# Performance work log

Measured on AMD Instinct MI355X. Metric: run time of the kernel, lower is better.

The kernel has to match this reference:

```python
import jax, jax.numpy as jnp
import numpy as np
import math

B, L, H, NH, DH = 2, 2048, 1024, 16, 64  # batch, seq, hidden, heads, head dim


def setup_inputs() -> dict:
    key = jax.random.key(0)
    ks = jax.random.split(key, 12)
    s = 0.02
    return {
        "v": jax.random.normal(ks[0], (B, L, H), jnp.float32),
        "k": jax.random.normal(ks[1], (B, L, H), jnp.float32),
        "q": jax.random.normal(ks[2], (B, L, H), jnp.float32),
        "mask": jnp.zeros((B, 1, 1, L), jnp.bool_),
        "Wv": jax.random.normal(ks[3], (H, H), jnp.float32) * s,
        "bv": jnp.zeros((H,), jnp.float32),
        "Wk": jax.random.normal(ks[4], (H, H), jnp.float32) * s,
        "bk": jnp.zeros((H,), jnp.float32),
        "Wq": jax.random.normal(ks[5], (H, H), jnp.float32) * s,
        "bq": jnp.zeros((H,), jnp.float32),
        "Wt": jax.random.normal(ks[6], (H, 1), jnp.float32) * s,
        "bt": jnp.zeros((1,), jnp.float32),
        "Wm": jax.random.normal(ks[7], (H, H), jnp.float32) * s,
        "bm": jnp.zeros((H,), jnp.float32),
    }


def reference(v, k, q, mask, Wv, bv, Wk, bk, Wq, bq, Wt, bt, Wm, bm):
    vp = (v @ Wv + bv).reshape(B, L, NH, DH).transpose(0, 2, 1, 3)  # [B,NH,L,DH]
    kp = k @ Wk + bk  # [B,L,H]
    qp = q @ Wq + bq  # [B,L,H]
    threshold = (qp * kp) @ Wt + bt  # [B,L,1] learned per-position gate threshold
    kh = kp.reshape(B, L, NH, DH).transpose(0, 2, 1, 3)  # [B,NH,L,DH]
    qh = qp.reshape(B, L, NH, DH).transpose(0, 2, 1, 3)
    scores = jnp.einsum("bhqd,bhkd->bhqk", qh, kh) / math.sqrt(DH)
    scores = jnp.where(mask, -1e9, scores)
    att_map = jax.nn.softmax(scores, axis=-1)  # [B,NH,Lq,Lk]
    # column sums: over queries (axis -2) then over heads -> [B,Lk,1]
    colsum = att_map.sum(axis=2).sum(axis=1)[..., None]
    a = (colsum - threshold) > 0  # [B,L,1] boolean gate
    atted = jnp.einsum("bhqk,bhkd->bhqd", att_map, vp)  # [B,NH,L,DH]
    atted = atted.transpose(0, 2, 1, 3).reshape(B, L, H)
    atted = atted * a.astype(atted.dtype)
    return atted @ Wm + bm
```

## Files before the change

### kernel.cpp

```cpp
#include <hip/hip_runtime.h>
#include <math.h>

#define BATCH 2
#define SEQ   2048
#define HID   1024
#define NHEAD 16
#define DHEAD 64
#define MROWS (BATCH*SEQ)
#define QK_SCALE 0.125f

typedef __attribute__((ext_vector_type(8))) short short8;
typedef __attribute__((ext_vector_type(4))) short short4v;
typedef __attribute__((ext_vector_type(4))) float floatx4;
#define MFMA16(a,b,c) __builtin_amdgcn_mfma_f32_16x16x32_bf16(a,b,c,0,0,0)

__device__ __forceinline__ unsigned short f2bf(float x) {
    union { float f; unsigned u; } v; v.f = x;
    return (unsigned short)((v.u + 0x8000u) >> 16);
}
__device__ __forceinline__ float bf2f(unsigned short s) {
    union { unsigned u; float f; } v; v.u = ((unsigned)s) << 16;
    return v.f;
}
__device__ __forceinline__ unsigned pack_bf16(float lo, float hi) {
    union { float f; unsigned u; } a, b; a.f = lo; b.f = hi;
    return __builtin_amdgcn_perm(b.u + 0x8000u, a.u + 0x8000u, 0x07060302u);
}

__global__ __launch_bounds__(256) void cvt_bf16_kernel(
    const float* __restrict__ i0, const float* __restrict__ i1,
    const float* __restrict__ i2,
    unsigned short* __restrict__ o0, unsigned short* __restrict__ o1,
    unsigned short* __restrict__ o2)
{
    const float* in; unsigned short* out;
    switch (blockIdx.y) {
        case 0:  in = i0; out = o0; break;
        case 1:  in = i1; out = o1; break;
        default: in = i2; out = o2; break;
    }
    const size_t i = ((size_t)blockIdx.x * 256 + threadIdx.x) * 8;
    const float4 a = *(const float4*)&in[i];
    const float4 b = *(const float4*)&in[i + 4];
    uint4 u;
    u.x = pack_bf16(a.x, a.y); u.y = pack_bf16(a.z, a.w);
    u.z = pack_bf16(b.x, b.y); u.w = pack_bf16(b.z, b.w);
    *(uint4*)&out[i] = u;
}

__global__ __launch_bounds__(256) void wtrans_kernel(
    const float* __restrict__ W0, const float* __restrict__ W1,
    const float* __restrict__ W2, const float* __restrict__ W3,
    unsigned short* __restrict__ T0, unsigned short* __restrict__ T1,
    unsigned short* __restrict__ T2, unsigned short* __restrict__ T3)
{
    const float* W; unsigned short* Wt;
    switch (blockIdx.z) {
        case 0: W = W0; Wt = T0; break;
        case 1: W = W1; Wt = T1; break;
        case 2: W = W2; Wt = T2; break;
        default: W = W3; Wt = T3; break;
    }
    __shared__ float T[64][68];
    const int tid = threadIdx.x;
    const int k0 = blockIdx.x * 64, n0 = blockIdx.y * 64;
#pragma unroll
    for (int it = 0; it < 4; it++) {
        const int id = it * 256 + tid;
        const int r = id >> 4, c4 = (id & 15) << 2;
        *(float4*)&T[r][c4] = *(const float4*)&W[(size_t)(k0 + r) * HID + n0 + c4];
    }
    __syncthreads();
#pragma unroll
    for (int it = 0; it < 2; it++) {
        const int id = it * 256 + tid;
        const int n = id >> 3, k8 = (id & 7) << 3;
        uint4 u;
        u.x = pack_bf16(T[k8 + 0][n], T[k8 + 1][n]);
        u.y = pack_bf16(T[k8 + 2][n], T[k8 + 3][n]);
        u.z = pack_bf16(T[k8 + 4][n], T[k8 + 5][n]);
        u.w = pack_bf16(T[k8 + 6][n], T[k8 + 7][n]);
        *(uint4*)&Wt[(size_t)(n0 + n) * HID + k0 + k8] = u;
    }
}

__global__ __launch_bounds__(256) void vtrans_kernel(
    const unsigned short* __restrict__ vb, unsigned short* __restrict__ vt)
{
    __shared__ unsigned short T[64][72];
    const int b = blockIdx.z, h = blockIdx.y, l0 = blockIdx.x * 64;
    const int tid = threadIdx.x;
#pragma unroll
    for (int it = 0; it < 2; it++) {
        const int id = it * 256 + tid;
        const int l = id >> 3, c8 = (id & 7) << 3;
        *(uint4*)&T[l][c8] =
            *(const uint4*)&vb[(size_t)(b * SEQ + l0 + l) * HID + h * DHEAD + c8];
    }
    __syncthreads();
#pragma unroll
    for (int it = 0; it < 2; it++) {
        const int id = it * 256 + tid;
        const int d = id >> 3, l8 = (id & 7) << 3;
        ushort4 u0, u1;
        u0.x = T[l8 + 0][d]; u0.y = T[l8 + 1][d];
        u0.z = T[l8 + 2][d]; u0.w = T[l8 + 3][d];
        u1.x = T[l8 + 4][d]; u1.y = T[l8 + 5][d];
        u1.z = T[l8 + 6][d]; u1.w = T[l8 + 7][d];
        const size_t o = ((size_t)(b * NHEAD + h) * DHEAD + d) * SEQ + l0 + l8;
        *(ushort4*)&vt[o] = u0;
        *(ushort4*)&vt[o + 4] = u1;
    }
}

__global__ __launch_bounds__(256) void gemm_mfma_kernel(
    const unsigned short* __restrict__ Ab, const unsigned short* __restrict__ Bt,
    const float* __restrict__ bias,
    const float* __restrict__ gate_cs, const float* __restrict__ gate_th,
    float* __restrict__ Cf, unsigned short* __restrict__ Cb,
    int M, int N, int K)
{
    __shared__ unsigned short As[128][72];
    __shared__ unsigned short Bs[128][72];
    const int tid = threadIdx.x;
    const int w = tid >> 6, lane = tid & 63;
    const int c = lane & 15, quad = lane >> 4;
    const int m0 = blockIdx.x * 128, n0 = blockIdx.y * 128;
    const int wm = (w >> 1) * 64, wn = (w & 1) * 64;

    bool grow[4] = {true, true, true, true};
    if (gate_cs) {
#pragma unroll
        for (int it = 0; it < 4; it++) {
            const int r = (it * 256 + tid) >> 3;
            grow[it] = (gate_cs[m0 + r] - gate_th[m0 + r]) > 0.f;
        }
    }

    floatx4 acc[4][4];
#pragma unroll
    for (int i = 0; i < 4; i++)
#pragma unroll
        for (int j = 0; j < 4; j++) acc[i][j] = (floatx4){0.f, 0.f, 0.f, 0.f};

    for (int kc = 0; kc < K; kc += 64) {
        __syncthreads();
#pragma unroll
        for (int it = 0; it < 4; it++) {
            const int id = it * 256 + tid;
            const int r = id >> 3, c8 = (id & 7) << 3;
            uint4 u = *(const uint4*)&Ab[(size_t)(m0 + r) * K + kc + c8];
            if (!grow[it]) { u.x = 0; u.y = 0; u.z = 0; u.w = 0; }
            *(uint4*)&As[r][c8] = u;
            *(uint4*)&Bs[r][c8] = *(const uint4*)&Bt[(size_t)(n0 + r) * K + kc + c8];
        }
        __syncthreads();
#pragma unroll
        for (int kk = 0; kk < 2; kk++) {
            short8 af[4], bf[4];
#pragma unroll
            for (int mt = 0; mt < 4; mt++)
                af[mt] = *(const short8*)&As[wm + mt * 16 + c][kk * 32 + quad * 8];
#pragma unroll
            for (int nt = 0; nt < 4; nt++)
                bf[nt] = *(const short8*)&Bs[wn + nt * 16 + c][kk * 32 + quad * 8];
#pragma unroll
            for (int mt = 0; mt < 4; mt++)
#pragma unroll
                for (int nt = 0; nt < 4; nt++)
                    acc[mt][nt] = MFMA16(af[mt], bf[nt], acc[mt][nt]);
        }
    }

#pragma unroll
    for (int nt = 0; nt < 4; nt++) {
        const int n = n0 + wn + nt * 16 + c;
        const float bb = bias[n];
#pragma unroll
        for (int mt = 0; mt < 4; mt++) {
            const int m = m0 + wm + mt * 16 + quad * 4;
#pragma unroll
            for (int r = 0; r < 4; r++) {
                const float val = acc[mt][nt][r] + bb;
                const size_t off = (size_t)(m + r) * N + n;
                if (Cf) Cf[off] = val;
                if (Cb) Cb[off] = f2bf(val);
            }
        }
    }
}

__global__ __launch_bounds__(256) void threshold_kernel(
    const unsigned short* __restrict__ qb, const unsigned short* __restrict__ kb,
    const float* __restrict__ Wt, const float* __restrict__ bt,
    float* __restrict__ thr)
{
    const int w = threadIdx.x >> 6, lane = threadIdx.x & 63;
    const int row = blockIdx.x * 4 + w;
    const unsigned short* qr = qb + (size_t)row * HID;
    const unsigned short* kr = kb + (size_t)row * HID;
    float s = 0.f;
#pragma unroll
    for (int ii = 0; ii < 2; ii++) {
        const int base = ii * 512 + lane * 8;
        const ushort4 q0 = *(const ushort4*)&qr[base];
        const ushort4 q1 = *(const ushort4*)&qr[base + 4];
        const ushort4 k0 = *(const ushort4*)&kr[base];
        const ushort4 k1 = *(const ushort4*)&kr[base + 4];
        const float4 w0 = *(const float4*)&Wt[base];
        const float4 w1 = *(const float4*)&Wt[base + 4];
        s += bf2f(q0.x) * bf2f(k0.x) * w0.x + bf2f(q0.y) * bf2f(k0.y) * w0.y +
             bf2f(q0.z) * bf2f(k0.z) * w0.z + bf2f(q0.w) * bf2f(k0.w) * w0.w +
             bf2f(q1.x) * bf2f(k1.x) * w1.x + bf2f(q1.y) * bf2f(k1.y) * w1.y +
             bf2f(q1.z) * bf2f(k1.z) * w1.z + bf2f(q1.w) * bf2f(k1.w) * w1.w;
    }
#pragma unroll
    for (int off = 32; off > 0; off >>= 1) s += __shfl_xor(s, off, 64);
    if (lane == 0) thr[row] = s + bt[0];
}

__global__ __launch_bounds__(512) void flash_mfma_kernel(
    const unsigned short* __restrict__ qb, const unsigned short* __restrict__ kb,
    const unsigned short* __restrict__ vt, const unsigned char* __restrict__ mask,
    unsigned short* __restrict__ att, float* __restrict__ zinv_out)
{
    const int b = blockIdx.z, h = blockIdx.y;
    const int q0 = blockIdx.x * 128;
    const int tid = threadIdx.x;
    const int w = tid >> 6, lane = tid & 63;
    const int c = lane & 15, quad = lane >> 4;

    __shared__ unsigned short Qs[128][72];
    __shared__ unsigned short Ks[64][72];
    __shared__ unsigned short Vs[64][72];
    __shared__ unsigned short Ps[8][16][68];
    __shared__ float mbf[64];

    const size_t hoff = (size_t)h * DHEAD;
#pragma unroll
    for (int it = 0; it < 2; it++) {
        const int g = it * 512 + tid;
        const int r = g >> 3, c8 = (g & 7) << 3;
        *(uint4*)&Qs[r][c8] =
            *(const uint4*)&qb[(size_t)(b * SEQ + q0 + r) * HID + hoff + c8];
    }
    __syncthreads();
    const short8 aq0 = *(const short8*)&Qs[w * 16 + c][quad * 8];
    const short8 aq1 = *(const short8*)&Qs[w * 16 + c][32 + quad * 8];

    floatx4 acc_o[4];
#pragma unroll
    for (int dt = 0; dt < 4; dt++) acc_o[dt] = (floatx4){0.f, 0.f, 0.f, 0.f};
    float zp[4] = {0.f, 0.f, 0.f, 0.f};
    const size_t vtbase = (size_t)(b * NHEAD + h) * DHEAD * SEQ;

    for (int kc = 0; kc < SEQ; kc += 64) {
        __syncthreads();
        {
            const int r = tid >> 3, c8 = (tid & 7) << 3;
            *(uint4*)&Ks[r][c8] =
                *(const uint4*)&kb[(size_t)(b * SEQ + kc + r) * HID + hoff + c8];
            *(uint4*)&Vs[r][c8] =
                *(const uint4*)&vt[vtbase + (size_t)r * SEQ + kc + c8];
        }
        if (tid < 64) mbf[tid] = mask[(size_t)b * SEQ + kc + tid] ? -1e9f : 0.f;
        __syncthreads();

#pragma unroll
        for (int nt = 0; nt < 4; nt++) {
            const short8 bk0 = *(const short8*)&Ks[nt * 16 + c][quad * 8];
            const short8 bk1 = *(const short8*)&Ks[nt * 16 + c][32 + quad * 8];
            floatx4 s = (floatx4){0.f, 0.f, 0.f, 0.f};
            s = MFMA16(aq0, bk0, s);
            s = MFMA16(aq1, bk1, s);
            const float mb = mbf[nt * 16 + c];
#pragma unroll
            for (int r = 0; r < 4; r++) {
                const float p = __expf(fmaf(s[r], QK_SCALE, mb));
                zp[r] += p;
                Ps[w][quad * 4 + r][nt * 16 + c] = f2bf(p);
            }
        }

        short4v p00 = *(const short4v*)&Ps[w][c][quad * 8];
        short4v p01 = *(const short4v*)&Ps[w][c][quad * 8 + 4];
        short4v p10 = *(const short4v*)&Ps[w][c][32 + quad * 8];
        short4v p11 = *(const short4v*)&Ps[w][c][32 + quad * 8 + 4];
        const short8 ap0 = __builtin_shufflevector(p00, p01, 0, 1, 2, 3, 4, 5, 6, 7);
        const short8 ap1 = __builtin_shufflevector(p10, p11, 0, 1, 2, 3, 4, 5, 6, 7);
#pragma unroll
        for (int dt = 0; dt < 4; dt++) {
            const short8 bv0 = *(const short8*)&Vs[dt * 16 + c][quad * 8];
            const short8 bv1 = *(const short8*)&Vs[dt * 16 + c][32 + quad * 8];
            acc_o[dt] = MFMA16(ap0, bv0, acc_o[dt]);
            acc_o[dt] = MFMA16(ap1, bv1, acc_o[dt]);
        }
    }

#pragma unroll
    for (int r = 0; r < 4; r++) {
        float z = zp[r];
        z += __shfl_xor(z, 1, 64); z += __shfl_xor(z, 2, 64);
        z += __shfl_xor(z, 4, 64); z += __shfl_xor(z, 8, 64);
        zp[r] = 1.0f / (z + 1e-30f);
    }

#pragma unroll
    for (int dt = 0; dt < 4; dt++)
#pragma unroll
        for (int r = 0; r < 4; r++)
            att[(size_t)(b * SEQ + q0 + w * 16 + quad * 4 + r) * HID + hoff +
                dt * 16 + c] = f2bf(acc_o[dt][r] * zp[r]);

    if (c == 0) {
        const size_t zb = (size_t)(b * NHEAD + h) * SEQ + q0 + w * 16 + quad * 4;
#pragma unroll
        for (int r = 0; r < 4; r++) zinv_out[zb + r] = zp[r];
    }
}

__global__ __launch_bounds__(512) void colsum_mfma_kernel(
    const unsigned short* __restrict__ qb, const unsigned short* __restrict__ kb,
    const unsigned char* __restrict__ mask, const float* __restrict__ zinv,
    float* __restrict__ colsum)
{
    const int b = blockIdx.z, h = blockIdx.y, k0 = blockIdx.x * 128;
    const int tid = threadIdx.x;
    const int w = tid >> 6, lane = tid & 63;
    const int c = lane & 15, quad = lane >> 4;

    __shared__ unsigned short Ks[128][72];
    __shared__ unsigned short Qs[64][72];
    __shared__ float zs[64];

    const size_t hoff = (size_t)h * DHEAD;
#pragma unroll
    for (int it = 0; it < 2; it++) {
        const int g = it * 512 + tid;
        const int r = g >> 3, c8 = (g & 7) << 3;
        *(uint4*)&Ks[r][c8] =
            *(const uint4*)&kb[(size_t)(b * SEQ + k0 + r) * HID + hoff + c8];
    }
    float mb[4];
#pragma unroll
    for (int r = 0; r < 4; r++)
        mb[r] = mask[(size_t)b * SEQ + k0 + w * 16 + quad * 4 + r] ? -1e9f : 0.f;
    __syncthreads();
    const short8 ak0 = *(const short8*)&Ks[w * 16 + c][quad * 8];
    const short8 ak1 = *(const short8*)&Ks[w * 16 + c][32 + quad * 8];

    float cs[4] = {0.f, 0.f, 0.f, 0.f};
    const size_t zbase = (size_t)(b * NHEAD + h) * SEQ;

    for (int qc = 0; qc < SEQ; qc += 64) {
        __syncthreads();
        {
            const int r = tid >> 3, c8 = (tid & 7) << 3;
            *(uint4*)&Qs[r][c8] =
                *(const uint4*)&qb[(size_t)(b * SEQ + qc + r) * HID + hoff + c8];
        }
        if (tid < 64) zs[tid] = zinv[zbase + qc + tid];
        __syncthreads();

#pragma unroll
        for (int qt = 0; qt < 4; qt++) {
            const short8 bq0 = *(const short8*)&Qs[qt * 16 + c][quad * 8];
            const short8 bq1 = *(const short8*)&Qs[qt * 16 + c][32 + quad * 8];
            floatx4 s = (floatx4){0.f, 0.f, 0.f, 0.f};
            s = MFMA16(ak0, bq0, s);
            s = MFMA16(ak1, bq1, s);
            const float zi = zs[qt * 16 + c];
#pragma unroll
            for (int r = 0; r < 4; r++)
                cs[r] += __expf(fmaf(s[r], QK_SCALE, mb[r])) * zi;
        }
    }

#pragma unroll
    for (int r = 0; r < 4; r++) {
        float v = cs[r];
        v += __shfl_xor(v, 1, 64); v += __shfl_xor(v, 2, 64);
        v += __shfl_xor(v, 4, 64); v += __shfl_xor(v, 8, 64);
        if (c == 0)
            atomicAdd(&colsum[(size_t)b * SEQ + k0 + w * 16 + quad * 4 + r], v);
    }
}

extern "C" void kernel_launch(void* const* d_in, const int* in_sizes, int n_in,
                              void* d_out, int out_size, void* d_ws, size_t ws_size,
                              hipStream_t stream)
{
    const float* v  = (const float*)d_in[0];
    const float* k  = (const float*)d_in[1];
    const float* q  = (const float*)d_in[2];
    const unsigned char* mask = (const unsigned char*)d_in[3];
    const float* Wv = (const float*)d_in[4];
    const float* bv = (const float*)d_in[5];
    const float* Wk = (const float*)d_in[6];
    const float* bk = (const float*)d_in[7];
    const float* Wq = (const float*)d_in[8];
    const float* bq = (const float*)d_in[9];
    const float* Wt = (const float*)d_in[10];
    const float* bt = (const float*)d_in[11];
    const float* Wm = (const float*)d_in[12];
    const float* bm = (const float*)d_in[13];
    float* out = (float*)d_out;

    const size_t NE = (size_t)MROWS * HID;
    const size_t WE = (size_t)HID * HID;
    unsigned short* qa   = (unsigned short*)d_ws;
    unsigned short* ka   = qa  + NE;
    unsigned short* va   = ka  + NE;
    unsigned short* qp   = va  + NE;
    unsigned short* kp   = qp  + NE;
    unsigned short* vp   = kp  + NE;
    unsigned short* WqT  = vp  + NE;
    unsigned short* WkT  = WqT + WE;
    unsigned short* WvT  = WkT + WE;
    unsigned short* WmT  = WvT + WE;
    float* thr    = (float*)(WmT + WE);
    float* zinv   = thr  + MROWS;
    float* colsum = zinv + (size_t)BATCH * NHEAD * SEQ;
    unsigned short* attb = qa;
    unsigned short* vtb  = ka;

    wtrans_kernel<<<dim3(HID / 64, HID / 64, 4), 256, 0, stream>>>(
        Wq, Wk, Wv, Wm, WqT, WkT, WvT, WmT);

    cvt_bf16_kernel<<<dim3((unsigned)(NE / (256 * 8)), 3), 256, 0, stream>>>(
        q, k, v, qa, ka, va);

    const dim3 gg(MROWS / 128, HID / 128);
    gemm_mfma_kernel<<<gg, 256, 0, stream>>>(qa, WqT, bq, nullptr, nullptr,
                                             nullptr, qp, MROWS, HID, HID);
    gemm_mfma_kernel<<<gg, 256, 0, stream>>>(ka, WkT, bk, nullptr, nullptr,
                                             nullptr, kp, MROWS, HID, HID);
    gemm_mfma_kernel<<<gg, 256, 0, stream>>>(va, WvT, bv, nullptr, nullptr,
                                             nullptr, vp, MROWS, HID, HID);

    vtrans_kernel<<<dim3(SEQ / 64, NHEAD, BATCH), 256, 0, stream>>>(vp, vtb);

    threshold_kernel<<<MROWS / 4, 256, 0, stream>>>(qp, kp, Wt, bt, thr);

    flash_mfma_kernel<<<dim3(SEQ / 128, NHEAD, BATCH), 512, 0, stream>>>(
        qp, kp, vtb, mask, attb, zinv);

    hipMemsetAsync(colsum, 0, MROWS * sizeof(float), stream);
    colsum_mfma_kernel<<<dim3(SEQ / 128, NHEAD, BATCH), 512, 0, stream>>>(
        qp, kp, mask, zinv, colsum);

    gemm_mfma_kernel<<<gg, 256, 0, stream>>>(attb, WmT, bm, colsum, thr,
                                             out, nullptr, MROWS, HID, HID);
}
```

Baseline: 340.9 us.

## Prefetch next tiles into registers, remap blocks per XCD, use native exp2

The GEMM, flash-attention and colsum kernels now load the next K/V/Q (and A/B) tile into registers while the current tile is being computed, so global-load latency overlaps the MFMA work. The flash and colsum kernels use a 1D grid with an XCD-aware remap, so blocks for the same (batch, head) land on the same XCD and can share L2 for K/V. The exponentials switch to native exp2 with the log2e factor folded into the scale. In exchange, register pressure rises, which could lower occupancy, and native exp2 is slightly less accurate.

```diff
diff --git a/kernel.cpp b/kernel.cpp
--- a/kernel.cpp
+++ b/kernel.cpp
@@ -8,11 +8,15 @@
 #define DHEAD 64
 #define MROWS (BATCH*SEQ)
 #define QK_SCALE 0.125f
+#define SCALE_LOG2E 0.1803368801111244f
 
 typedef __attribute__((ext_vector_type(8))) short short8;
 typedef __attribute__((ext_vector_type(4))) short short4v;
 typedef __attribute__((ext_vector_type(4))) float floatx4;
 #define MFMA16(a,b,c) __builtin_amdgcn_mfma_f32_16x16x32_bf16(a,b,c,0,0,0)
+
+extern "C" __device__ float __ocml_native_exp2_f32(float);
+#define EXP2F(x) __ocml_native_exp2_f32(x)
 
 __device__ __forceinline__ unsigned short f2bf(float x) {
     union { float f; unsigned u; } v; v.f = x;
@@ -143,18 +147,36 @@
 #pragma unroll
         for (int j = 0; j < 4; j++) acc[i][j] = (floatx4){0.f, 0.f, 0.f, 0.f};
 
+    uint4 ra[4], rb[4];
+#pragma unroll
+    for (int it = 0; it < 4; it++) {
+        const int id = it * 256 + tid;
+        const int r = id >> 3, c8 = (id & 7) << 3;
+        ra[it] = *(const uint4*)&Ab[(size_t)(m0 + r) * K + c8];
+        rb[it] = *(const uint4*)&Bt[(size_t)(n0 + r) * K + c8];
+    }
+
     for (int kc = 0; kc < K; kc += 64) {
         __syncthreads();
 #pragma unroll
         for (int it = 0; it < 4; it++) {
             const int id = it * 256 + tid;
             const int r = id >> 3, c8 = (id & 7) << 3;
-            uint4 u = *(const uint4*)&Ab[(size_t)(m0 + r) * K + kc + c8];
+            uint4 u = ra[it];
             if (!grow[it]) { u.x = 0; u.y = 0; u.z = 0; u.w = 0; }
             *(uint4*)&As[r][c8] = u;
-            *(uint4*)&Bs[r][c8] = *(const uint4*)&Bt[(size_t)(n0 + r) * K + kc + c8];
-        }
-        __syncthreads();
+            *(uint4*)&Bs[r][c8] = rb[it];
+        }
+        __syncthreads();
+        if (kc + 64 < K) {
+#pragma unroll
+            for (int it = 0; it < 4; it++) {
+                const int id = it * 256 + tid;
+                const int r = id >> 3, c8 = (id & 7) << 3;
+                ra[it] = *(const uint4*)&Ab[(size_t)(m0 + r) * K + kc + 64 + c8];
+                rb[it] = *(const uint4*)&Bt[(size_t)(n0 + r) * K + kc + 64 + c8];
+            }
+        }
 #pragma unroll
         for (int kk = 0; kk < 2; kk++) {
             short8 af[4], bf[4];
@@ -224,8 +246,13 @@
     const unsigned short* __restrict__ vt, const unsigned char* __restrict__ mask,
     unsigned short* __restrict__ att, float* __restrict__ zinv_out)
 {
-    const int b = blockIdx.z, h = blockIdx.y;
-    const int q0 = blockIdx.x * 128;
+    const int n = blockIdx.x;
+    const int xcd = n & 7, t = n >> 3;
+    const int g = xcd + 8 * (t >> 4);
+    const int qblk = t & 15;
+    const int h = g & 15, b = g >> 4;
+    const int q0 = qblk * 128;
+
     const int tid = threadIdx.x;
     const int w = tid >> 6, lane = tid & 63;
     const int c = lane & 15, quad = lane >> 4;
@@ -239,8 +266,8 @@
     const size_t hoff = (size_t)h * DHEAD;
 #pragma unroll
     for (int it = 0; it < 2; it++) {
-        const int g = it * 512 + tid;
-        const int r = g >> 3, c8 = (g & 7) << 3;
+        const int gg = it * 512 + tid;
+        const int r = gg >> 3, c8 = (gg & 7) << 3;
         *(uint4*)&Qs[r][c8] =
             *(const uint4*)&qb[(size_t)(b * SEQ + q0 + r) * HID + hoff + c8];
     }
@@ -254,17 +281,23 @@
     float zp[4] = {0.f, 0.f, 0.f, 0.f};
     const size_t vtbase = (size_t)(b * NHEAD + h) * DHEAD * SEQ;
 
+    const int sr = tid >> 3, sc8 = (tid & 7) << 3;
+    uint4 kreg = *(const uint4*)&kb[(size_t)(b * SEQ + sr) * HID + hoff + sc8];
+    uint4 vreg = *(const uint4*)&vt[vtbase + (size_t)sr * SEQ + sc8];
+    float mreg = 0.f;
+    if (tid < 64) mreg = mask[(size_t)b * SEQ + tid] ? -1e9f : 0.f;
+
     for (int kc = 0; kc < SEQ; kc += 64) {
         __syncthreads();
-        {
-            const int r = tid >> 3, c8 = (tid & 7) << 3;
-            *(uint4*)&Ks[r][c8] =
-                *(const uint4*)&kb[(size_t)(b * SEQ + kc + r) * HID + hoff + c8];
-            *(uint4*)&Vs[r][c8] =
-                *(const uint4*)&vt[vtbase + (size_t)r * SEQ + kc + c8];
-        }
-        if (tid < 64) mbf[tid] = mask[(size_t)b * SEQ + kc + tid] ? -1e9f : 0.f;
-        __syncthreads();
+        *(uint4*)&Ks[sr][sc8] = kreg;
+        *(uint4*)&Vs[sr][sc8] = vreg;
+        if (tid < 64) mbf[tid] = mreg;
+        __syncthreads();
+        if (kc + 64 < SEQ) {
+            kreg = *(const uint4*)&kb[(size_t)(b * SEQ + kc + 64 + sr) * HID + hoff + sc8];
+            vreg = *(const uint4*)&vt[vtbase + (size_t)sr * SEQ + kc + 64 + sc8];
+            if (tid < 64) mreg = mask[(size_t)b * SEQ + kc + 64 + tid] ? -1e9f : 0.f;
+        }
 
 #pragma unroll
         for (int nt = 0; nt < 4; nt++) {
@@ -276,7 +309,7 @@
             const float mb = mbf[nt * 16 + c];
 #pragma unroll
             for (int r = 0; r < 4; r++) {
-                const float p = __expf(fmaf(s[r], QK_SCALE, mb));
+                const float p = EXP2F(fmaf(s[r], SCALE_LOG2E, mb));
                 zp[r] += p;
                 Ps[w][quad * 4 + r][nt * 16 + c] = f2bf(p);
             }
@@ -324,7 +357,12 @@
     const unsigned char* __restrict__ mask, const float* __restrict__ zinv,
     float* __restrict__ colsum)
 {
-    const int b = blockIdx.z, h = blockIdx.y, k0 = blockIdx.x * 128;
+    const int n = blockIdx.x;
+    const int xcd = n & 7, t = n >> 3;
+    const int g = xcd + 8 * (t >> 4);
+    const int h = g & 15, b = g >> 4;
+    const int k0 = (t & 15) * 128;
+
     const int tid = threadIdx.x;
     const int w = tid >> 6, lane = tid & 63;
     const int c = lane & 15, quad = lane >> 4;
@@ -336,8 +374,8 @@
     const size_t hoff = (size_t)h * DHEAD;
 #pragma unroll
     for (int it = 0; it < 2; it++) {
-        const int g = it * 512 + tid;
-        const int r = g >> 3, c8 = (g & 7) << 3;
+        const int gg = it * 512 + tid;
+        const int r = gg >> 3, c8 = (gg & 7) << 3;
         *(uint4*)&Ks[r][c8] =
             *(const uint4*)&kb[(size_t)(b * SEQ + k0 + r) * HID + hoff + c8];
     }
@@ -352,15 +390,22 @@
     float cs[4] = {0.f, 0.f, 0.f, 0.f};
     const size_t zbase = (size_t)(b * NHEAD + h) * SEQ;
 
+    const int sr = tid >> 3, sc8 = (tid & 7) << 3;
+    uint4 qreg; float zreg = 0.f;
+    if (tid < 512) {
+        qreg = *(const uint4*)&qb[(size_t)(b * SEQ + sr) * HID + hoff + sc8];
+        if (tid < 64) zreg = zinv[zbase + tid];
+    }
+
     for (int qc = 0; qc < SEQ; qc += 64) {
         __syncthreads();
-        {
-            const int r = tid >> 3, c8 = (tid & 7) << 3;
-            *(uint4*)&Qs[r][c8] =
-                *(const uint4*)&qb[(size_t)(b * SEQ + qc + r) * HID + hoff + c8];
-        }
-        if (tid < 64) zs[tid] = zinv[zbase + qc + tid];
-        __syncthreads();
+        *(uint4*)&Qs[sr][sc8] = qreg;
+        if (tid < 64) zs[tid] = zreg;
+        __syncthreads();
+        if (qc + 64 < SEQ) {
+            qreg = *(const uint4*)&qb[(size_t)(b * SEQ + qc + 64 + sr) * HID + hoff + sc8];
+            if (tid < 64) zreg = zinv[zbase + qc + 64 + tid];
+        }
 
 #pragma unroll
         for (int qt = 0; qt < 4; qt++) {
@@ -372,7 +417,7 @@
             const float zi = zs[qt * 16 + c];
 #pragma unroll
             for (int r = 0; r < 4; r++)
-                cs[r] += __expf(fmaf(s[r], QK_SCALE, mb[r])) * zi;
+                cs[r] += EXP2F(fmaf(s[r], SCALE_LOG2E, mb[r])) * zi;
         }
     }
 
@@ -442,11 +487,11 @@
 
     threshold_kernel<<<MROWS / 4, 256, 0, stream>>>(qp, kp, Wt, bt, thr);
 
-    flash_mfma_kernel<<<dim3(SEQ / 128, NHEAD, BATCH), 512, 0, stream>>>(
+    flash_mfma_kernel<<<BATCH * NHEAD * (SEQ / 128), 512, 0, stream>>>(
         qp, kp, vtb, mask, attb, zinv);
 
     hipMemsetAsync(colsum, 0, MROWS * sizeof(float), stream);
-    colsum_mfma_kernel<<<dim3(SEQ / 128, NHEAD, BATCH), 512, 0, stream>>>(
+    colsum_mfma_kernel<<<BATCH * NHEAD * (SEQ / 128), 512, 0, stream>>>(
         qp, kp, mask, zinv, colsum);
 
     gemm_mfma_kernel<<<gg, 256, 0, stream>>>(attb, WmT, bm, colsum, thr,
```

New measurement: 354.8 us. 1.04x slower.
